# Kernel tuning notes

Measured on AMD Instinct MI355X. Metric: run time of the kernel, lower is better.

Reference implementation:

```python
import jax, jax.numpy as jnp
import numpy as np

L = 4        # num_blocks
D = 512      # d_model
H = 8        # num_heads
DFF = 2048   # d_ff
EPS = 1.1920929e-07  # torch RMSNorm default eps = finfo(fp32).eps


def setup_inputs() -> dict:
    key = jax.random.key(0)
    ks = jax.random.split(key, 12)
    B, S = 4, 1024
    s = 0.02
    return {
        "x": jax.random.normal(ks[0], (B, S, D), jnp.float32),
        "col_ids": jax.random.randint(ks[1], (B, S), 0, 32),
        "row_ids": jax.random.randint(ks[2], (B, S), 0, 128),
        "nbr_ids": jax.random.randint(ks[3], (B, S), 0, 64),
        # per-block, per-relation attention weights (nn.Linear: y = x @ W.T)
        "Wq": jax.random.normal(ks[4], (L, 4, D, D), jnp.float32) * s,
        "Wk": jax.random.normal(ks[5], (L, 4, D, D), jnp.float32) * s,
        "Wv": jax.random.normal(ks[6], (L, 4, D, D), jnp.float32) * s,
        "Wo": jax.random.normal(ks[7], (L, 4, D, D), jnp.float32) * s,
        # SwiGLU FFN weights per block
        "W1": jax.random.normal(ks[8], (L, DFF, D), jnp.float32) * s,
        "W3": jax.random.normal(ks[9], (L, DFF, D), jnp.float32) * s,
        "W2": jax.random.normal(ks[10], (L, D, DFF), jnp.float32) * s,
        # RMSNorm scales: 4 attn norms + 1 ffn norm per block + final norm_out
        "g_attn": jnp.ones((L, 4, D), jnp.float32),
        "g_ffn": jnp.ones((L, D), jnp.float32),
        "g_out": jnp.ones((D,), jnp.float32),
    }


def _rms(x, g):
    return x * jax.lax.rsqrt(jnp.mean(x * x, axis=-1, keepdims=True) + EPS) * g


def _attn(x, wq, wk, wv, wo, mask):
    # x: [B,S,D]; mask: [B,S,S] bool (True = attend) or None for full attention
    B, S, _ = x.shape
    hd = D // H
    scale = 1.0 / np.sqrt(hd).astype(np.float32)
    q = (x @ wq.T).reshape(B, S, H, hd).transpose(0, 2, 1, 3)  # bhsd
    k = (x @ wk.T).reshape(B, S, H, hd).transpose(0, 2, 1, 3)
    v = (x @ wv.T).reshape(B, S, H, hd).transpose(0, 2, 1, 3)
    sc = jnp.einsum('bhqd,bhkd->bhqk', q, k) * scale
    if mask is not None:
        sc = jnp.where(mask[:, None, :, :], sc, jnp.float32(-1e30))
    a = jax.nn.softmax(sc, axis=-1)
    o = jnp.einsum('bhqk,bhkd->bhqd', a, v).transpose(0, 2, 1, 3).reshape(B, S, D)
    return o @ wo.T


def reference(x, col_ids, row_ids, nbr_ids, Wq, Wk, Wv, Wo, W1, W3, W2, g_attn, g_ffn, g_out):
    # relation order in RelationalBlock: col, feat, nbr, full
    masks = [ids[:, :, None] == ids[:, None, :] for ids in (col_ids, row_ids, nbr_ids)] + [None]
    for l in range(L):
        for r in range(4):
            x = x + _attn(_rms(x, g_attn[l, r]), Wq[l, r], Wk[l, r], Wv[l, r], Wo[l, r], masks[r])
        h = _rms(x, g_ffn[l])
        x = x + (jax.nn.silu(h @ W1[l].T) * (h @ W3[l].T)) @ W2[l].T
    return _rms(x, g_out)
```

## Files before the change

kernel.cpp:

```cpp
#include <hip/hip_runtime.h>
#include <hip/hip_bf16.h>


typedef __attribute__((ext_vector_type(4))) float f32x4;
typedef __attribute__((ext_vector_type(8))) short s16x8;
typedef __attribute__((ext_vector_type(4))) short s16x4;
typedef __attribute__((ext_vector_type(4))) unsigned u32x4;
typedef __attribute__((ext_vector_type(2))) unsigned u32x2;

#define SEQ 1024
#define DM 512
#define MTOT 4096
#define EPSV 1.1920929e-07f
#define LOG2E 1.44269504088896f

static __device__ __forceinline__ float b2f(short s) {
  unsigned u = ((unsigned)(unsigned short)s) << 16;
  return __builtin_bit_cast(float, u);
}
static __device__ __forceinline__ short f2b(float f) {
  unsigned u = __builtin_bit_cast(unsigned, f);
  u = (u + 0x7fffu + ((u >> 16) & 1u)) >> 16;
  return (short)(unsigned short)u;
}
static __device__ __forceinline__ unsigned cvtpk(float lo, float hi) {
  unsigned r;
  asm("v_cvt_pk_bf16_f32 %0, %1, %2" : "=v"(r) : "v"(lo), "v"(hi));
  return r;
}

#define MFMA_BF16(a, b, c) __builtin_amdgcn_mfma_f32_16x16x32_bf16((a), (b), (c), 0, 0, 0)
#define GLLDS(gp, lp)                                                                        \
  __builtin_amdgcn_global_load_lds((const __attribute__((address_space(1))) unsigned*)(gp),  \
                                   (__attribute__((address_space(3))) unsigned*)(lp), 16, 0, 0)
#define GLLDS4(gp, lp)                                                                       \
  __builtin_amdgcn_global_load_lds((const __attribute__((address_space(1))) unsigned*)(gp),  \
                                   (__attribute__((address_space(3))) unsigned*)(lp), 4, 0, 0)

__global__ void cvt_all(const f32x4* __restrict__ wq, const f32x4* __restrict__ wk,
                        const f32x4* __restrict__ wv, const f32x4* __restrict__ wo,
                        const f32x4* __restrict__ w1, const f32x4* __restrict__ w3,
                        const f32x4* __restrict__ w2, const float* __restrict__ g_attn,
                        const float* __restrict__ g_ffn, s16x4* __restrict__ wqkv,
                        s16x4* __restrict__ wob, s16x4* __restrict__ w13,
                        s16x4* __restrict__ w2b, const float* __restrict__ xin,
                        float* __restrict__ x, short* __restrict__ h,
                        float* __restrict__ sbuf) {
  int i = blockIdx.x * 256 + threadIdx.x;
  int which = blockIdx.y;
  s16x4 o;
  if (which < 3) {
    const f32x4* src = which == 0 ? wq : (which == 1 ? wk : wv);
    f32x4 v = src[i];
    int lr = i >> 16, k4 = i & 127, n = (i >> 7) & 511;
    const float* gp = g_attn + lr * 512 + k4 * 4;
    float sc = (which == 0) ? 0.125f * LOG2E : 1.0f;
#pragma unroll
    for (int j = 0; j < 4; j++) o[j] = f2b(v[j] * gp[j] * sc);
    wqkv[(size_t)lr * 196608 + (which * 512 + n) * 128 + k4] = o;
  } else if (which == 3) {
    f32x4 v = wo[i];
#pragma unroll
    for (int j = 0; j < 4; j++) o[j] = f2b(v[j]);
    wob[i] = o;
  } else if (which < 6) {
    const f32x4* src = which == 4 ? w1 : w3;
    int off = which - 4;
    f32x4 v = src[i];
    int l = i >> 18, n = (i >> 7) & 2047, k4 = i & 127;
    const float* gp = g_ffn + l * 512 + k4 * 4;
#pragma unroll
    for (int j = 0; j < 4; j++) o[j] = f2b(v[j] * gp[j]);
    w13[(size_t)l * 524288 + (n * 2 + off) * 128 + k4] = o;
  } else if (which == 6) {
    f32x4 v = w2[i];
#pragma unroll
    for (int j = 0; j < 4; j++) o[j] = f2b(v[j]);
    w2b[i] = o;
  } else {
    if (blockIdx.x >= 1024) return;
    int gid = blockIdx.x * 256 + threadIdx.x;
    if (gid < 20 * 4096) sbuf[4096 + gid] = 0.f;
    int row = blockIdx.x * 4 + (threadIdx.x >> 6);
    int lane = threadIdx.x & 63;
    const float* xr = xin + (size_t)row * DM + lane * 8;
    f32x4 a = *(const f32x4*)xr;
    f32x4 b = *(const f32x4*)(xr + 4);
    float* xo = x + (size_t)row * DM + lane * 8;
    *(f32x4*)xo = a;
    *(f32x4*)(xo + 4) = b;
    s16x8 ho;
#pragma unroll
    for (int j = 0; j < 4; j++) { ho[j] = f2b(a[j]); ho[4 + j] = f2b(b[j]); }
    *(s16x8*)(h + (size_t)row * DM + lane * 8) = ho;
    float ss = a[0]*a[0]+a[1]*a[1]+a[2]*a[2]+a[3]*a[3]+b[0]*b[0]+b[1]*b[1]+b[2]*b[2]+b[3]*b[3];
#pragma unroll
    for (int m = 1; m < 64; m <<= 1) ss += __shfl_xor(ss, m, 64);
    if (lane == 0) sbuf[row] = ss;
  }
}

__global__ void rmsnorm_out(const float* __restrict__ x, const float* __restrict__ g,
                            float* __restrict__ outp) {
  int row = blockIdx.x * 4 + (threadIdx.x >> 6);
  int lane = threadIdx.x & 63;
  const float* xr = x + (size_t)row * DM + lane * 8;
  f32x4 a = *(const f32x4*)xr;
  f32x4 b = *(const f32x4*)(xr + 4);
  float ss = a[0]*a[0]+a[1]*a[1]+a[2]*a[2]+a[3]*a[3]+b[0]*b[0]+b[1]*b[1]+b[2]*b[2]+b[3]*b[3];
#pragma unroll
  for (int m = 1; m < 64; m <<= 1) ss += __shfl_xor(ss, m, 64);
  float sc = rsqrtf(ss * (1.0f / DM) + EPSV);
  const float* gp = g + lane * 8;
  float* o = outp + (size_t)row * DM + lane * 8;
  f32x4 o0, o1;
#pragma unroll
  for (int j = 0; j < 4; j++) { o0[j] = a[j] * sc * gp[j]; o1[j] = b[j] * sc * gp[4 + j]; }
  *(f32x4*)o = o0;
  *(f32x4*)(o + 4) = o1;
}

template<int AR, int AC, int FUSE>
__global__ __launch_bounds__(256) void gemm_bt(const short* __restrict__ A, const short* __restrict__ W,
                                               short* __restrict__ outb, float* __restrict__ outf,
                                               short* __restrict__ vtb,
                                               const float* __restrict__ ssq_in,
                                               float* __restrict__ ssq_out,
                                               short* __restrict__ hb, int N, int K) {
  constexpr int BM = AR * 32;
  constexpr int BN = AC * 32;
  constexpr int NA = BM / 64, NB = BN / 64;
  constexpr int LPS = NA + NB;
  __shared__ short As[2][BM * 32];
  __shared__ short Bs[2][BN * 32];
  const int tid = threadIdx.x;
  const int lane = tid & 63;
  const int w = tid >> 6;
  const int wr = w >> 1, wc = w & 1;
  const int qi = lane & 15, g = lane >> 4;
  const int m0 = blockIdx.x * BM, n0 = blockIdx.y * BN;

  const short* ap[NA];
  const short* wp[NB];
#pragma unroll
  for (int i = 0; i < NA; i++) {
    int s = i * 256 + tid;
    int row = s >> 2, gl = s & 3, gd = gl ^ ((row >> 1) & 3);
    ap[i] = A + (size_t)(m0 + row) * K + gd * 8;
  }
#pragma unroll
  for (int i = 0; i < NB; i++) {
    int s = i * 256 + tid;
    int row = s >> 2, gl = s & 3, gd = gl ^ ((row >> 1) & 3);
    wp[i] = W + (size_t)(n0 + row) * K + gd * 8;
  }
  int aro[AR], bro[AC];
#pragma unroll
  for (int i = 0; i < AR; i++) {
    int row = wr * AR * 16 + i * 16 + qi;
    aro[i] = row * 64 + ((g ^ ((row >> 1) & 3)) * 16);
  }
#pragma unroll
  for (int j = 0; j < AC; j++) {
    int row = wc * AC * 16 + j * 16 + qi;
    bro[j] = row * 64 + ((g ^ ((row >> 1) & 3)) * 16);
  }
  f32x4 acc[AR][AC] = {};

#define STAGE_G(BUF)                                                             \
  {                                                                              \
    _Pragma("unroll")                                                            \
    for (int i = 0; i < NA; i++) {                                               \
      GLLDS(ap[i], (char*)As[BUF] + (i * 256 + w * 64) * 16);                    \
      ap[i] += 32;                                                               \
    }                                                                            \
    _Pragma("unroll")                                                            \
    for (int i = 0; i < NB; i++) {                                               \
      GLLDS(wp[i], (char*)Bs[BUF] + (i * 256 + w * 64) * 16);                    \
      wp[i] += 32;                                                               \
    }                                                                            \
  }

#define BODY_G(BUF, T)                                                           \
  {                                                                              \
    s16x8 af[AR], bf[AC];                                                        \
    _Pragma("unroll")                                                            \
    for (int i = 0; i < AR; i++) af[i] = *(const s16x8*)((char*)As[BUF] + aro[i]); \
    _Pragma("unroll")                                                            \
    for (int j = 0; j < AC; j++) bf[j] = *(const s16x8*)((char*)Bs[BUF] + bro[j]); \
    asm volatile("s_waitcnt lgkmcnt(0)" ::: "memory");                           \
    __builtin_amdgcn_s_barrier();                                                \
    bool more = ((T) + 2 < nt);                                                  \
    if (more) STAGE_G(BUF);                                                      \
    _Pragma("unroll")                                                            \
    for (int i = 0; i < AR; i++)                                                 \
      _Pragma("unroll")                                                          \
      for (int j = 0; j < AC; j++)                                               \
        acc[i][j] = MFMA_BF16(af[i], bf[j], acc[i][j]);                          \
    if (more) asm volatile("s_waitcnt vmcnt(%0)" :: "n"(LPS) : "memory");        \
    else      asm volatile("s_waitcnt vmcnt(0)" ::: "memory");                   \
    __builtin_amdgcn_s_barrier();                                                \
  }

  const int nt = K >> 5;
  STAGE_G(0);
  STAGE_G(1);
  asm volatile("s_waitcnt vmcnt(%0)" :: "n"(LPS) : "memory");
  __builtin_amdgcn_s_barrier();
  for (int t = 0; t < nt; t += 2) {
    BODY_G(0, t);
    BODY_G(1, t + 1);
  }
#undef STAGE_G
#undef BODY_G

  float srow[AR][4];
  if (FUSE == 2 || FUSE == 3) {
#pragma unroll
    for (int i = 0; i < AR; i++) {
      int rbase = m0 + wr * AR * 16 + i * 16 + g * 4;
#pragma unroll
      for (int r = 0; r < 4; r++)
        srow[i][r] = rsqrtf(ssq_in[rbase + r] * (1.0f / DM) + EPSV);
    }
  }
  float part[AR][4];
  if (FUSE == 1) {
#pragma unroll
    for (int i = 0; i < AR; i++)
#pragma unroll
      for (int r = 0; r < 4; r++) part[i][r] = 0.f;
  }

#pragma unroll
  for (int i = 0; i < AR; i++) {
    int rbase = m0 + wr * AR * 16 + i * 16 + g * 4;
#pragma unroll
    for (int j = 0; j < AC; j++) {
      int col = n0 + wc * AC * 16 + j * 16 + qi;
      if (FUSE == 2 && col >= 1024) {
        int bbv = rbase >> 10, s = rbase & 1023;
        int c = col - 1024, hhv = c >> 6, d = c & 63;
        int o = (s & 63) >> 2;
        int gg = o & 3, h2 = (o >> 2) & 1, q32 = o >> 3;
        int pnew = q32 * 8 + gg * 2 + h2;
        u32x2 ov;
        ov[0] = cvtpk(acc[i][j][0] * srow[i][0], acc[i][j][1] * srow[i][1]);
        ov[1] = cvtpk(acc[i][j][2] * srow[i][2], acc[i][j][3] * srow[i][3]);
        *(s16x4*)(vtb + (((size_t)(bbv * 8 + hhv) * 64 + d) << 10) + (s & ~63) + pnew * 4) =
            __builtin_bit_cast(s16x4, ov);
      } else if (FUSE == 3) {
#pragma unroll
        for (int r = 0; r < 4; r++) {
          float own = acc[i][j][r] * srow[i][r];
          float other = __shfl_xor(own, 1, 64);
          float sv = own / (1.0f + __expf(-own));
          if (!(lane & 1))
            outb[(size_t)(rbase + r) * (N >> 1) + (col >> 1)] = f2b(sv * other);
        }
      } else if (FUSE == 1) {
#pragma unroll
        for (int r = 0; r < 4; r++) {
          size_t idx = (size_t)(rbase + r) * N + col;
          float xnew = outf[idx] + acc[i][j][r];
          outf[idx] = xnew;
          hb[idx] = f2b(xnew);
          part[i][r] += xnew * xnew;
        }
      } else {
#pragma unroll
        for (int r = 0; r < 4; r++)
          outb[(size_t)(rbase + r) * N + col] = f2b(acc[i][j][r] * srow[i][r]);
      }
    }
  }
  if (FUSE == 1) {
#pragma unroll
    for (int i = 0; i < AR; i++) {
      int rbase = m0 + wr * AR * 16 + i * 16 + g * 4;
#pragma unroll
      for (int r = 0; r < 4; r++) {
        float p = part[i][r];
#pragma unroll
        for (int m = 1; m < 16; m <<= 1) p += __shfl_xor(p, m, 16);
        if (qi == 0) atomicAdd(&ssq_out[rbase + r], p);
      }
    }
  }
}

__global__ __launch_bounds__(256) void attn_kernel(const short* __restrict__ qkv, const short* __restrict__ vt,
                                                   const int* __restrict__ ids, short* __restrict__ Ob) {
  const int bh = blockIdx.x;
  const int bb = bh >> 3, hh = bh & 7;
  const int q0 = blockIdx.y * 64;
  const int tid = threadIdx.x, lane = tid & 63, w = tid >> 6;
  const int g = lane >> 4, qi = lane & 15;
  __shared__ short Kl[2][128 * 64];
  __shared__ short Vl[2][64 * 128];
  __shared__ int Kid[2][128];
  const short* kbase = qkv + 512 + hh * 64;
  const short* vbase = vt + (size_t)bh * 64 * SEQ;
  s16x8 qf0, qf1;
  {
    int qrow = q0 + w * 16 + qi;
    const short* qp = qkv + (size_t)(bb * SEQ + qrow) * 1536 + hh * 64 + g * 8;
    qf0 = *(const s16x8*)qp;
    qf1 = *(const s16x8*)(qp + 32);
  }
  int qid = 0;
  if (ids) qid = ids[bb * SEQ + q0 + w * 16 + qi];
  float m_ = -1e30f, l_ = 0.f;
  f32x4 oacc[4] = {};

#define STAGE_ATTN(buf, ktt)                                                                     \
  {                                                                                              \
    _Pragma("unroll")                                                                            \
    for (int i = 0; i < 4; i++) {                                                                \
      int s = i * 256 + tid;                                                                     \
      int row = s >> 3, gl = s & 7, gd = gl ^ (row & 7);                                         \
      GLLDS(kbase + (size_t)(bb * SEQ + (ktt) + row) * 1536 + gd * 8,                            \
            (char*)Kl[buf] + (i * 256 + w * 64) * 16);                                           \
    }                                                                                            \
    _Pragma("unroll")                                                                            \
    for (int i = 0; i < 4; i++) {                                                                \
      int s = i * 256 + tid;                                                                     \
      int d = s >> 4, gl = s & 15, gd = gl ^ (d & 7);                                            \
      GLLDS(vbase + (size_t)d * SEQ + (ktt) + gd * 8, (char*)Vl[buf] + (i * 256 + w * 64) * 16); \
    }                                                                                            \
    if (ids && w < 2) GLLDS4(ids + bb * SEQ + (ktt) + w * 64 + lane, (char*)Kid[buf] + w * 256); \
  }

  STAGE_ATTN(0, 0);
  __syncthreads();
  int cur = 0;
  for (int kt = 0; kt < SEQ; kt += 128) {
    if (kt + 128 < SEQ) STAGE_ATTN(cur ^ 1, kt + 128);
    f32x4 sc[8];
#pragma unroll
    for (int kc = 0; kc < 8; kc++) {
      int krow = kc * 16 + qi;
      s16x8 kf0 = *(const s16x8*)(Kl[cur] + krow * 64 + ((g ^ (krow & 7)) * 8));
      s16x8 kf1 = *(const s16x8*)(Kl[cur] + krow * 64 + (((4 + g) ^ (krow & 7)) * 8));
      f32x4 s4 = {};
      s4 = MFMA_BF16(kf0, qf0, s4);
      s4 = MFMA_BF16(kf1, qf1, s4);
      sc[kc] = s4;
    }
    float p[8][4];
#pragma unroll
    for (int kc = 0; kc < 8; kc++)
#pragma unroll
      for (int r = 0; r < 4; r++) p[kc][r] = sc[kc][r];
    if (ids) {
#pragma unroll
      for (int kc = 0; kc < 8; kc++) {
        int4 kid4 = *(const int4*)(Kid[cur] + kc * 16 + g * 4);
        if (kid4.x != qid) p[kc][0] = -1e30f;
        if (kid4.y != qid) p[kc][1] = -1e30f;
        if (kid4.z != qid) p[kc][2] = -1e30f;
        if (kid4.w != qid) p[kc][3] = -1e30f;
      }
    }
    float mx = fmaxf(fmaxf(p[0][0], p[0][1]), fmaxf(p[0][2], p[0][3]));
#pragma unroll
    for (int kc = 1; kc < 8; kc++)
      mx = fmaxf(mx, fmaxf(fmaxf(p[kc][0], p[kc][1]), fmaxf(p[kc][2], p[kc][3])));
    mx = fmaxf(mx, __shfl_xor(mx, 16, 64));
    mx = fmaxf(mx, __shfl_xor(mx, 32, 64));
    if (__any(mx > m_ + 8.f)) {
      float nm = fmaxf(m_, mx);
      float c = exp2f(m_ - nm);
      m_ = nm;
      l_ *= c;
#pragma unroll
      for (int r = 0; r < 4; r++) {
        float cr = __shfl(c, g * 4 + r, 16);
        oacc[0][r] *= cr; oacc[1][r] *= cr; oacc[2][r] *= cr; oacc[3][r] *= cr;
      }
    }
    float sum = 0.f;
#pragma unroll
    for (int kc = 0; kc < 8; kc++)
#pragma unroll
      for (int r = 0; r < 4; r++) {
        p[kc][r] = exp2f(p[kc][r] - m_);
        sum += p[kc][r];
      }
    sum += __shfl_xor(sum, 16, 64);
    sum += __shfl_xor(sum, 32, 64);
    l_ += sum;
#pragma unroll
    for (int kk = 0; kk < 2; kk++) {
      u32x4 ua, ub;
      ua[0] = cvtpk(p[kk * 4 + 0][0], p[kk * 4 + 0][1]);
      ua[1] = cvtpk(p[kk * 4 + 0][2], p[kk * 4 + 0][3]);
      ua[2] = cvtpk(p[kk * 4 + 1][0], p[kk * 4 + 1][1]);
      ua[3] = cvtpk(p[kk * 4 + 1][2], p[kk * 4 + 1][3]);
      ub[0] = cvtpk(p[kk * 4 + 2][0], p[kk * 4 + 2][1]);
      ub[1] = cvtpk(p[kk * 4 + 2][2], p[kk * 4 + 2][3]);
      ub[2] = cvtpk(p[kk * 4 + 3][0], p[kk * 4 + 3][1]);
      ub[3] = cvtpk(p[kk * 4 + 3][2], p[kk * 4 + 3][3]);
      s16x8 pa = __builtin_bit_cast(s16x8, ua);
      s16x8 pb = __builtin_bit_cast(s16x8, ub);
#pragma unroll
      for (int dt = 0; dt < 4; dt++) {
        int dl = dt * 16 + qi;
        const short* vr = Vl[cur] + dl * 128;
        s16x8 vf0 = *(const s16x8*)(vr + (kk * 8 + (g ^ (dl & 7))) * 8);
        s16x8 vf1 = *(const s16x8*)(vr + (kk * 8 + ((4 + g) ^ (dl & 7))) * 8);
        oacc[dt] = MFMA_BF16(pa, vf0, oacc[dt]);
        oacc[dt] = MFMA_BF16(pb, vf1, oacc[dt]);
      }
    }
    __syncthreads();
    cur ^= 1;
  }
#undef STAGE_ATTN
  const size_t obase = (size_t)(bb * SEQ) * DM + hh * 64;
#pragma unroll
  for (int r = 0; r < 4; r++) {
    float lr = __shfl(l_, g * 4 + r, 16);
    float inv = 1.0f / lr;
    int q = q0 + w * 16 + g * 4 + r;
#pragma unroll
    for (int dt = 0; dt < 4; dt++)
      Ob[obase + (size_t)q * DM + dt * 16 + qi] = f2b(oacc[dt][r] * inv);
  }
}

extern "C" void kernel_launch(void* const* d_in, const int* in_sizes, int n_in,
                              void* d_out, int out_size, void* d_ws, size_t ws_size,
                              hipStream_t stream) {
  const float* x_in  = (const float*)d_in[0];
  const int* col_ids = (const int*)d_in[1];
  const int* row_ids = (const int*)d_in[2];
  const int* nbr_ids = (const int*)d_in[3];
  const float* g_attn = (const float*)d_in[11];
  const float* g_ffn  = (const float*)d_in[12];
  const float* g_out  = (const float*)d_in[13];

  char* ws = (char*)d_ws;
  float* x    = (float*)(ws);
  short* h    = (short*)(ws + (size_t)(8u  << 20));
  short* qkv  = (short*)(ws + (size_t)(12u << 20));
  short* vt   = (short*)(ws + (size_t)(24u << 20));
  short* ob   = (short*)(ws + (size_t)(28u << 20));
  float* sbuf = (float*)(ws + (size_t)(33u << 20));
  short* fa   = (short*)(ws + (size_t)(44u << 20));
  short* wqkv = (short*)(ws + (size_t)(60u  << 20));
  short* wob  = (short*)(ws + (size_t)(84u  << 20));
  short* w13  = (short*)(ws + (size_t)(92u  << 20));
  short* w2b  = (short*)(ws + (size_t)(108u << 20));

  cvt_all<<<dim3(4096, 8), 256, 0, stream>>>((const f32x4*)d_in[4], (const f32x4*)d_in[5],
                                             (const f32x4*)d_in[6], (const f32x4*)d_in[7],
                                             (const f32x4*)d_in[8], (const f32x4*)d_in[9],
                                             (const f32x4*)d_in[10], g_attn, g_ffn,
                                             (s16x4*)wqkv, (s16x4*)wob, (s16x4*)w13, (s16x4*)w2b,
                                             x_in, x, h, sbuf);

  const int* idsarr[4] = {col_ids, row_ids, nbr_ids, nullptr};

  for (int l = 0; l < 4; l++) {
    for (int r = 0; r < 4; r++) {
      int slot = l * 5 + r;
      size_t woff = (size_t)(l * 4 + r) * 1536 * DM;
      gemm_bt<4, 2, 2><<<dim3(32, 24), 256, 0, stream>>>(h, wqkv + woff, qkv, nullptr, vt,
                                                         sbuf + (size_t)slot * 4096, nullptr,
                                                         nullptr, 1536, DM);
      attn_kernel<<<dim3(32, 16), 256, 0, stream>>>(qkv, vt, idsarr[r], ob);
      gemm_bt<2, 2, 1><<<dim3(64, 8), 256, 0, stream>>>(ob, wob + (size_t)(l * 4 + r) * DM * DM,
                                                        nullptr, x, nullptr, nullptr,
                                                        sbuf + (size_t)(slot + 1) * 4096, h, DM, DM);
    }
    int fslot = l * 5 + 4;
    gemm_bt<4, 2, 3><<<dim3(32, 64), 256, 0, stream>>>(h, w13 + (size_t)l * 4096 * DM, fa, nullptr,
                                                       nullptr, sbuf + (size_t)fslot * 4096,
                                                       nullptr, nullptr, 4096, DM);
    gemm_bt<2, 2, 1><<<dim3(64, 8), 256, 0, stream>>>(fa, w2b + (size_t)l * DM * 2048, nullptr, x,
                                                      nullptr, nullptr,
                                                      sbuf + (size_t)(fslot + 1) * 4096, h, DM, 2048);
  }
  rmsnorm_out<<<1024, 256, 0, stream>>>(x, g_out, (float*)d_out);
}
```

Baseline: 1.100 ms.

## Load attention K/V/ids directly from global memory instead of LDS staging

Removes the double-buffered LDS staging of K, V and key ids in the attention kernel, along with the per-tile barriers. Each wave now loads its MFMA fragments straight from global memory and relies on L1/L2 caching. This frees LDS and drops synchronisation, which may raise occupancy. In exchange, the four waves in a block fetch the same K/V data redundantly, and the loads are no longer prefetched ahead of the compute, so latency is more exposed.

New measurement: 1.830 ms. 1.66x slower.

```diff
diff --git a/kernel.cpp b/kernel.cpp
--- a/kernel.cpp
+++ b/kernel.cpp
@@ -33,9 +33,6 @@
 #define GLLDS(gp, lp)                                                                        \
   __builtin_amdgcn_global_load_lds((const __attribute__((address_space(1))) unsigned*)(gp),  \
                                    (__attribute__((address_space(3))) unsigned*)(lp), 16, 0, 0)
-#define GLLDS4(gp, lp)                                                                       \
-  __builtin_amdgcn_global_load_lds((const __attribute__((address_space(1))) unsigned*)(gp),  \
-                                   (__attribute__((address_space(3))) unsigned*)(lp), 4, 0, 0)
 
 __global__ void cvt_all(const f32x4* __restrict__ wq, const f32x4* __restrict__ wk,
                         const f32x4* __restrict__ wv, const f32x4* __restrict__ wo,
@@ -296,11 +293,6 @@
   const int q0 = blockIdx.y * 64;
   const int tid = threadIdx.x, lane = tid & 63, w = tid >> 6;
   const int g = lane >> 4, qi = lane & 15;
-  __shared__ short Kl[2][128 * 64];
-  __shared__ short Vl[2][64 * 128];
-  __shared__ int Kid[2][128];
-  const short* kbase = qkv + 512 + hh * 64;
-  const short* vbase = vt + (size_t)bh * 64 * SEQ;
   s16x8 qf0, qf1;
   {
     int qrow = q0 + w * 16 + qi;
@@ -313,35 +305,17 @@
   float m_ = -1e30f, l_ = 0.f;
   f32x4 oacc[4] = {};
 
-#define STAGE_ATTN(buf, ktt)                                                                     \
-  {                                                                                              \
-    _Pragma("unroll")                                                                            \
-    for (int i = 0; i < 4; i++) {                                                                \
-      int s = i * 256 + tid;                                                                     \
-      int row = s >> 3, gl = s & 7, gd = gl ^ (row & 7);                                         \
-      GLLDS(kbase + (size_t)(bb * SEQ + (ktt) + row) * 1536 + gd * 8,                            \
-            (char*)Kl[buf] + (i * 256 + w * 64) * 16);                                           \
-    }                                                                                            \
-    _Pragma("unroll")                                                                            \
-    for (int i = 0; i < 4; i++) {                                                                \
-      int s = i * 256 + tid;                                                                     \
-      int d = s >> 4, gl = s & 15, gd = gl ^ (d & 7);                                            \
-      GLLDS(vbase + (size_t)d * SEQ + (ktt) + gd * 8, (char*)Vl[buf] + (i * 256 + w * 64) * 16); \
-    }                                                                                            \
-    if (ids && w < 2) GLLDS4(ids + bb * SEQ + (ktt) + w * 64 + lane, (char*)Kid[buf] + w * 256); \
-  }
-
-  STAGE_ATTN(0, 0);
-  __syncthreads();
-  int cur = 0;
+  const short* kb = qkv + (size_t)(bb * SEQ + qi) * 1536 + 512 + hh * 64 + g * 8;
+  const short* vb = vt + ((size_t)bh * 64 + qi) * SEQ + g * 8;
+  const int* idb = ids ? ids + bb * SEQ + g * 4 : nullptr;
+
   for (int kt = 0; kt < SEQ; kt += 128) {
-    if (kt + 128 < SEQ) STAGE_ATTN(cur ^ 1, kt + 128);
     f32x4 sc[8];
 #pragma unroll
     for (int kc = 0; kc < 8; kc++) {
-      int krow = kc * 16 + qi;
-      s16x8 kf0 = *(const s16x8*)(Kl[cur] + krow * 64 + ((g ^ (krow & 7)) * 8));
-      s16x8 kf1 = *(const s16x8*)(Kl[cur] + krow * 64 + (((4 + g) ^ (krow & 7)) * 8));
+      const short* kp = kb + (size_t)(kt + kc * 16) * 1536;
+      s16x8 kf0 = *(const s16x8*)kp;
+      s16x8 kf1 = *(const s16x8*)(kp + 32);
       f32x4 s4 = {};
       s4 = MFMA_BF16(kf0, qf0, s4);
       s4 = MFMA_BF16(kf1, qf1, s4);
@@ -355,7 +329,7 @@
     if (ids) {
 #pragma unroll
       for (int kc = 0; kc < 8; kc++) {
-        int4 kid4 = *(const int4*)(Kid[cur] + kc * 16 + g * 4);
+        int4 kid4 = *(const int4*)(idb + kt + kc * 16);
         if (kid4.x != qid) p[kc][0] = -1e30f;
         if (kid4.y != qid) p[kc][1] = -1e30f;
         if (kid4.z != qid) p[kc][2] = -1e30f;
@@ -405,18 +379,14 @@
       s16x8 pb = __builtin_bit_cast(s16x8, ub);
 #pragma unroll
       for (int dt = 0; dt < 4; dt++) {
-        int dl = dt * 16 + qi;
-        const short* vr = Vl[cur] + dl * 128;
-        s16x8 vf0 = *(const s16x8*)(vr + (kk * 8 + (g ^ (dl & 7))) * 8);
-        s16x8 vf1 = *(const s16x8*)(vr + (kk * 8 + ((4 + g) ^ (dl & 7))) * 8);
+        const short* vp = vb + (size_t)(dt * 16) * SEQ + kt + kk * 64;
+        s16x8 vf0 = *(const s16x8*)vp;
+        s16x8 vf1 = *(const s16x8*)(vp + 32);
         oacc[dt] = MFMA_BF16(pa, vf0, oacc[dt]);
         oacc[dt] = MFMA_BF16(pb, vf1, oacc[dt]);
       }
     }
-    __syncthreads();
-    cur ^= 1;
-  }
-#undef STAGE_ATTN
+  }
   const size_t obase = (size_t)(bb * SEQ) * DM + hh * 64;
 #pragma unroll
   for (int r = 0; r < 4; r++) {
```
